# Performance work log

Hardware: AMD Instinct MI355X
Metric: run time of the kernel (lower is better)

Reference implementation:

```python
import jax, jax.numpy as jnp
import numpy as np

B, D, K = 65536, 128, 8
BOUND = 3.0
MIN_BIN_W = 1e-3   # min_bin_width
MIN_BIN_H = 1e-3   # min_bin_height
MIN_DERIV = 1e-3   # min_derivative
EPS = 1e-6


def setup_inputs() -> dict:
    key = jax.random.key(0)
    k1, k2, k3, k4 = jax.random.split(key, 4)
    return {
        "x": jax.random.normal(k1, (B, D), jnp.float32) * 1.5,
        "unnormalized_widths": jax.random.normal(k2, (D, K), jnp.float32),
        "unnormalized_heights": jax.random.normal(k3, (D, K), jnp.float32),
        "unnormalized_derivatives": jax.random.normal(k4, (D, K - 1), jnp.float32),
    }


def _calculate_knots(lengths, lower, upper):
    # lengths: [D, K] summing to ~1 -> scaled lengths and knot positions [D, K+1]
    knots = jnp.cumsum(lengths, axis=-1)
    knots = jnp.pad(knots, ((0, 0), (1, 0)))
    knots = (upper - lower) * knots + lower
    knots = knots.at[..., 0].set(lower)
    knots = knots.at[..., -1].set(upper)
    return knots[..., 1:] - knots[..., :-1], knots


def _select_bins(p, idx):
    # p: [D, Kp] per-dim tables, idx: [B, D] bin indices -> [B, D]
    i = jnp.clip(idx, 0, p.shape[-1] - 1)
    return p[jnp.arange(p.shape[0])[None, :], i]


def _spline_forward(x, uw, uh, ud):
    w = jax.nn.softmax(uw, axis=-1)
    h = jax.nn.softmax(uh, axis=-1)
    d = jax.nn.softplus(ud)

    num_bins = w.shape[-1]
    widths = MIN_BIN_W + (1.0 - MIN_BIN_W * num_bins) * w
    heights = MIN_BIN_H + (1.0 - MIN_BIN_H * num_bins) * h
    derivs = jnp.pad(MIN_DERIV + d, ((0, 0), (1, 1)), constant_values=1.0 - MIN_DERIV)  # [D, K+1]

    widths, cumwidths = _calculate_knots(widths, -BOUND, BOUND)
    heights, cumheights = _calculate_knots(heights, -BOUND, BOUND)

    inside = (x >= -BOUND) & (x <= BOUND)
    xc = jnp.clip(x, -BOUND, BOUND)  # keep tail values finite; masked out below

    # searchsorted: which bin each input falls into   [B, D]
    bin_idx = jnp.sum(xc[..., None] >= (cumwidths + EPS)[None, :, :], axis=-1) - 1

    iw = _select_bins(widths, bin_idx)
    icw = _select_bins(cumwidths, bin_idx)
    ich = _select_bins(cumheights, bin_idx)
    idelta = _select_bins(heights / widths, bin_idx)
    id0 = _select_bins(derivs, bin_idx)
    id1 = _select_bins(derivs[..., 1:], bin_idx)
    ih = _select_bins(heights, bin_idx)

    # rational quadratic spline (forward)
    theta = (xc - icw) / iw
    t1m = theta * (1.0 - theta)
    numerator = ih * (idelta * theta ** 2 + id0 * t1m)
    denominator = idelta + (id0 + id1 - 2.0 * idelta) * t1m
    out = ich + numerator / denominator
    dnum = idelta ** 2 * (id1 * theta ** 2 + 2.0 * idelta * t1m + id0 * (1.0 - theta) ** 2)
    lad = jnp.log(dnum) - 2.0 * jnp.log(denominator)

    u = jnp.where(inside, out, x)          # identity outside tail bound
    lad = jnp.where(inside, lad, 0.0)
    return u, lad


def reference(x, unnormalized_widths, unnormalized_heights, unnormalized_derivatives):
    u, lad = _spline_forward(x, unnormalized_widths, unnormalized_heights, unnormalized_derivatives)
    log_detJ = jnp.sum(lad, axis=1)
    return u, log_detJ
```

## Files before the change

### kernel.cpp

```cpp
#include <hip/hip_runtime.h>
#include <math.h>

namespace {
constexpr int D = 128;
constexpr int K = 8;
constexpr float BOUND = 3.0f;
constexpr float EPS = 1e-6f;
constexpr float MIN_BIN_W = 1e-3f;
constexpr float MIN_BIN_H = 1e-3f;
constexpr float MIN_DERIV = 1e-3f;
constexpr float LN2 = 0.6931471805599453f;
constexpr int WPB = 8;
constexpr int RPW = 8;
}

typedef float v2f __attribute__((ext_vector_type(2)));

template <int CTRL, int ROWM>
__device__ __forceinline__ float dpp_add(float v) {
    const int t = __builtin_amdgcn_update_dpp(0, __float_as_int(v), CTRL, ROWM, 0xf, true);
    return v + __int_as_float(t);
}

__device__ __forceinline__ float wave_sum_dpp(float v) {
    v = dpp_add<0x111, 0xf>(v);
    v = dpp_add<0x112, 0xf>(v);
    v = dpp_add<0x114, 0xf>(v);
    v = dpp_add<0x118, 0xf>(v);
    v = dpp_add<0x142, 0xa>(v);
    v = dpp_add<0x143, 0xc>(v);
    return v;
}

__global__ __launch_bounds__(512, 6) void spline_fwd(
    const float* __restrict__ x,
    const float* __restrict__ uw,
    const float* __restrict__ uh,
    const float* __restrict__ ud,
    float* __restrict__ out_u,
    float* __restrict__ out_ld,
    int nrows)
{
    __shared__ __align__(16) float4 s_T[2 * K * D];

    const int tid = threadIdx.x;
    if (tid < D) {
        const int d = tid;
        float wv[K], hv[K], cw[K + 1], ch[K + 1], der[K + 1];

        {
            const float* p = uw + d * K;
            float m = p[0];
            #pragma unroll
            for (int j = 1; j < K; ++j) m = fmaxf(m, p[j]);
            float s = 0.f;
            #pragma unroll
            for (int j = 0; j < K; ++j) { wv[j] = __expf(p[j] - m); s += wv[j]; }
            const float inv = (1.f - MIN_BIN_W * K) / s;
            #pragma unroll
            for (int j = 0; j < K; ++j) wv[j] = MIN_BIN_W + wv[j] * inv;
        }
        {
            const float* p = uh + d * K;
            float m = p[0];
            #pragma unroll
            for (int j = 1; j < K; ++j) m = fmaxf(m, p[j]);
            float s = 0.f;
            #pragma unroll
            for (int j = 0; j < K; ++j) { hv[j] = __expf(p[j] - m); s += hv[j]; }
            const float inv = (1.f - MIN_BIN_H * K) / s;
            #pragma unroll
            for (int j = 0; j < K; ++j) hv[j] = MIN_BIN_H + hv[j] * inv;
        }
        cw[0] = -BOUND; ch[0] = -BOUND;
        float cs_w = 0.f, cs_h = 0.f;
        #pragma unroll
        for (int j = 0; j < K; ++j) {
            cs_w += wv[j]; cw[j + 1] = 2.f * BOUND * cs_w - BOUND;
            cs_h += hv[j]; ch[j + 1] = 2.f * BOUND * cs_h - BOUND;
        }
        cw[K] = BOUND; ch[K] = BOUND;

        der[0] = 1.f - MIN_DERIV;
        der[K] = 1.f - MIN_DERIV;
        {
            const float* p = ud + d * (K - 1);
            #pragma unroll
            for (int j = 1; j < K; ++j) {
                const float v = p[j - 1];
                const float sp = log1pf(__expf(-fabsf(v))) + fmaxf(v, 0.f);
                der[j] = MIN_DERIV + sp;
            }
        }

        const int slot = (d & 1) * 64 + (d >> 1);
        #pragma unroll
        for (int j = 0; j < K; ++j) {
            const float w  = cw[j + 1] - cw[j];
            const float h  = ch[j + 1] - ch[j];
            const float iw = 1.f / w;
            const float dl = h * iw;
            s_T[j * D + slot] = make_float4(cw[j], iw, der[j], dl);
            s_T[K * D + j * D + slot] = make_float4(ch[j], h, der[j + 1],
                                                    der[j] + der[j + 1] - 2.f * dl);
        }
    }
    __syncthreads();

    const int wave = tid >> 6;
    const int lane = tid & 63;
    const int slot0 = lane;
    const int slot1 = 64 + lane;
    const float4* __restrict__ pa0 = s_T + slot0;
    const float4* __restrict__ pa1 = s_T + slot1;

    float kn0[7], kn1[7];
    #pragma unroll
    for (int j = 0; j < 7; ++j) {
        kn0[j] = pa0[(j + 1) * D].x + EPS;
        kn1[j] = pa1[(j + 1) * D].x + EPS;
    }

    const int r0 = (blockIdx.x * WPB + wave) * RPW;
    const int lo2 = lane * 2;
    const float* __restrict__ xbase = x + (size_t)r0 * D + lo2;
    float* __restrict__ ubase = out_u + (size_t)r0 * D + lo2;

    float2 xs[RPW];
    #pragma unroll
    for (int i = 0; i < RPW; ++i)
        xs[i] = *(const float2*)(xbase + (size_t)i * D);

    #pragma unroll
    for (int i = 0; i < RPW; ++i) {
        const float xv0 = xs[i].x, xv1 = xs[i].y;
        const float xc0 = fminf(fmaxf(xv0, -BOUND), BOUND);
        const float xc1 = fminf(fmaxf(xv1, -BOUND), BOUND);
        const bool in0 = fabsf(xv0) <= BOUND;
        const bool in1 = fabsf(xv1) <= BOUND;

        int i0 = 0, i1 = 0;
        #pragma unroll
        for (int j = 0; j < 7; ++j) {
            i0 += (xc0 >= kn0[j]) ? 1 : 0;
            i1 += (xc1 >= kn1[j]) ? 1 : 0;
        }

        const float4 ra0 = pa0[i0 * D];
        const float4 rb0 = pa0[i0 * D + K * D];
        const float4 ra1 = pa1[i1 * D];
        const float4 rb1 = pa1[i1 * D + K * D];

        const v2f xc  = {xc0, xc1};
        const v2f xw  = {xv0, xv1};
        const v2f icw = {ra0.x, ra1.x}, inw = {ra0.y, ra1.y};
        const v2f d0  = {ra0.z, ra1.z}, dl  = {ra0.w, ra1.w};
        const v2f ich = {rb0.x, rb1.x}, ih  = {rb0.y, rb1.y};
        const v2f d1  = {rb0.z, rb1.z}, E   = {rb0.w, rb1.w};

        const v2f theta = (xc - icw) * inw;
        const v2f omt   = (v2f)1.f - theta;
        const v2f t1m   = theta * omt;
        const v2f th2   = theta * theta;
        const v2f num   = ih * (dl * th2 + d0 * t1m);
        const v2f den   = dl + E * t1m;
        const v2f rd    = {__builtin_amdgcn_rcpf(den.x), __builtin_amdgcn_rcpf(den.y)};
        const v2f outv  = num * rd + ich;
        const v2f dnum  = (dl * dl) * (d1 * th2 + (dl + dl) * t1m + d0 * (omt * omt));
        const v2f P     = dnum * (rd * rd);

        const v2f u = outv + (xw - xc);
        *(float2*)(ubase + (size_t)i * D) = make_float2(u.x, u.y);

        const float P0 = in0 ? P.x : 1.f;
        const float P1 = in1 ? P.y : 1.f;
        float la = __log2f(P0 * P1);

        la = wave_sum_dpp(la);
        if (lane == 63) out_ld[r0 + i] = la * LN2;
    }
}

extern "C" void kernel_launch(void* const* d_in, const int* in_sizes, int n_in,
                              void* d_out, int out_size, void* d_ws, size_t ws_size,
                              hipStream_t stream) {
    const float* x  = (const float*)d_in[0];
    const float* uw = (const float*)d_in[1];
    const float* uh = (const float*)d_in[2];
    const float* ud = (const float*)d_in[3];
    const int nrows = in_sizes[0] / D;
    float* out_u  = (float*)d_out;
    float* out_ld = (float*)d_out + (size_t)nrows * D;
    const int nblocks = nrows / (WPB * RPW);
    spline_fwd<<<nblocks, 512, 0, stream>>>(x, uw, uh, ud, out_u, out_ld, nrows);
}
```

Measured before the change: 96.29 us.

## Process four dims per lane with float4 I/O and half-wave row reduction

Result: no change. 96.33 us (+0.0%).

```diff
diff --git a/kernel.cpp b/kernel.cpp
--- a/kernel.cpp
+++ b/kernel.cpp
@@ -22,17 +22,16 @@
     return v + __int_as_float(t);
 }
 
-__device__ __forceinline__ float wave_sum_dpp(float v) {
+__device__ __forceinline__ float half_sum_dpp(float v) {
     v = dpp_add<0x111, 0xf>(v);
     v = dpp_add<0x112, 0xf>(v);
     v = dpp_add<0x114, 0xf>(v);
     v = dpp_add<0x118, 0xf>(v);
     v = dpp_add<0x142, 0xa>(v);
-    v = dpp_add<0x143, 0xc>(v);
     return v;
 }
 
-__global__ __launch_bounds__(512, 6) void spline_fwd(
+__global__ __launch_bounds__(512, 4) void spline_fwd(
     const float* __restrict__ x,
     const float* __restrict__ uw,
     const float* __restrict__ uh,
@@ -93,7 +92,7 @@
             }
         }
 
-        const int slot = (d & 1) * 64 + (d >> 1);
+        const int slot = (d & 3) * 32 + (d >> 2);
         #pragma unroll
         for (int j = 0; j < K; ++j) {
             const float w  = cw[j + 1] - cw[j];
@@ -109,75 +108,90 @@
 
     const int wave = tid >> 6;
     const int lane = tid & 63;
-    const int slot0 = lane;
-    const int slot1 = 64 + lane;
-    const float4* __restrict__ pa0 = s_T + slot0;
-    const float4* __restrict__ pa1 = s_T + slot1;
-
-    float kn0[7], kn1[7];
+    const int l32  = lane & 31;
+    const int rsel = lane >> 5;
+
+    const float4* __restrict__ pa0 = s_T + (0 * 32 + l32);
+    const float4* __restrict__ pa1 = s_T + (1 * 32 + l32);
+    const float4* __restrict__ pa2 = s_T + (2 * 32 + l32);
+    const float4* __restrict__ pa3 = s_T + (3 * 32 + l32);
+
+    float kn0[7], kn1[7], kn2[7], kn3[7];
     #pragma unroll
     for (int j = 0; j < 7; ++j) {
         kn0[j] = pa0[(j + 1) * D].x + EPS;
         kn1[j] = pa1[(j + 1) * D].x + EPS;
+        kn2[j] = pa2[(j + 1) * D].x + EPS;
+        kn3[j] = pa3[(j + 1) * D].x + EPS;
     }
 
     const int r0 = (blockIdx.x * WPB + wave) * RPW;
-    const int lo2 = lane * 2;
-    const float* __restrict__ xbase = x + (size_t)r0 * D + lo2;
-    float* __restrict__ ubase = out_u + (size_t)r0 * D + lo2;
-
-    float2 xs[RPW];
+    const float* __restrict__ xbase = x + (size_t)(r0 + rsel) * D + l32 * 4;
+    float* __restrict__ ubase = out_u + (size_t)(r0 + rsel) * D + l32 * 4;
+
+    float4 xs[4];
     #pragma unroll
-    for (int i = 0; i < RPW; ++i)
-        xs[i] = *(const float2*)(xbase + (size_t)i * D);
+    for (int i = 0; i < 4; ++i)
+        xs[i] = *(const float4*)(xbase + (size_t)(2 * i) * D);
 
     #pragma unroll
-    for (int i = 0; i < RPW; ++i) {
-        const float xv0 = xs[i].x, xv1 = xs[i].y;
-        const float xc0 = fminf(fmaxf(xv0, -BOUND), BOUND);
-        const float xc1 = fminf(fmaxf(xv1, -BOUND), BOUND);
-        const bool in0 = fabsf(xv0) <= BOUND;
-        const bool in1 = fabsf(xv1) <= BOUND;
-
-        int i0 = 0, i1 = 0;
+    for (int i = 0; i < 4; ++i) {
+        const float4 xv = xs[i];
+        const float xc0 = fminf(fmaxf(xv.x, -BOUND), BOUND);
+        const float xc1 = fminf(fmaxf(xv.y, -BOUND), BOUND);
+        const float xc2 = fminf(fmaxf(xv.z, -BOUND), BOUND);
+        const float xc3 = fminf(fmaxf(xv.w, -BOUND), BOUND);
+
+        int i0 = 0, i1 = 0, i2 = 0, i3 = 0;
         #pragma unroll
         for (int j = 0; j < 7; ++j) {
             i0 += (xc0 >= kn0[j]) ? 1 : 0;
             i1 += (xc1 >= kn1[j]) ? 1 : 0;
-        }
-
-        const float4 ra0 = pa0[i0 * D];
-        const float4 rb0 = pa0[i0 * D + K * D];
-        const float4 ra1 = pa1[i1 * D];
-        const float4 rb1 = pa1[i1 * D + K * D];
-
-        const v2f xc  = {xc0, xc1};
-        const v2f xw  = {xv0, xv1};
-        const v2f icw = {ra0.x, ra1.x}, inw = {ra0.y, ra1.y};
-        const v2f d0  = {ra0.z, ra1.z}, dl  = {ra0.w, ra1.w};
-        const v2f ich = {rb0.x, rb1.x}, ih  = {rb0.y, rb1.y};
-        const v2f d1  = {rb0.z, rb1.z}, E   = {rb0.w, rb1.w};
-
-        const v2f theta = (xc - icw) * inw;
-        const v2f omt   = (v2f)1.f - theta;
-        const v2f t1m   = theta * omt;
-        const v2f th2   = theta * theta;
-        const v2f num   = ih * (dl * th2 + d0 * t1m);
-        const v2f den   = dl + E * t1m;
-        const v2f rd    = {__builtin_amdgcn_rcpf(den.x), __builtin_amdgcn_rcpf(den.y)};
-        const v2f outv  = num * rd + ich;
-        const v2f dnum  = (dl * dl) * (d1 * th2 + (dl + dl) * t1m + d0 * (omt * omt));
-        const v2f P     = dnum * (rd * rd);
-
-        const v2f u = outv + (xw - xc);
-        *(float2*)(ubase + (size_t)i * D) = make_float2(u.x, u.y);
-
-        const float P0 = in0 ? P.x : 1.f;
-        const float P1 = in1 ? P.y : 1.f;
-        float la = __log2f(P0 * P1);
-
-        la = wave_sum_dpp(la);
-        if (lane == 63) out_ld[r0 + i] = la * LN2;
+            i2 += (xc2 >= kn2[j]) ? 1 : 0;
+            i3 += (xc3 >= kn3[j]) ? 1 : 0;
+        }
+
+        const float4 ra0 = pa0[i0 * D], rb0 = pa0[i0 * D + K * D];
+        const float4 ra1 = pa1[i1 * D], rb1 = pa1[i1 * D + K * D];
+        const float4 ra2 = pa2[i2 * D], rb2 = pa2[i2 * D + K * D];
+        const float4 ra3 = pa3[i3 * D], rb3 = pa3[i3 * D + K * D];
+
+        const v2f xcA = {xc0, xc1},  xcB = {xc2, xc3};
+        const v2f xwA = {xv.x, xv.y}, xwB = {xv.z, xv.w};
+        const v2f icwA = {ra0.x, ra1.x}, icwB = {ra2.x, ra3.x};
+        const v2f inwA = {ra0.y, ra1.y}, inwB = {ra2.y, ra3.y};
+        const v2f d0A  = {ra0.z, ra1.z}, d0B  = {ra2.z, ra3.z};
+        const v2f dlA  = {ra0.w, ra1.w}, dlB  = {ra2.w, ra3.w};
+        const v2f ichA = {rb0.x, rb1.x}, ichB = {rb2.x, rb3.x};
+        const v2f ihA  = {rb0.y, rb1.y}, ihB  = {rb2.y, rb3.y};
+        const v2f d1A  = {rb0.z, rb1.z}, d1B  = {rb2.z, rb3.z};
+        const v2f EA   = {rb0.w, rb1.w}, EB   = {rb2.w, rb3.w};
+
+        const v2f thA = (xcA - icwA) * inwA,      thB = (xcB - icwB) * inwB;
+        const v2f omA = (v2f)1.f - thA,           omB = (v2f)1.f - thB;
+        const v2f tmA = thA * omA,                tmB = thB * omB;
+        const v2f t2A = thA * thA,                t2B = thB * thB;
+        const v2f nmA = ihA * (dlA * t2A + d0A * tmA);
+        const v2f nmB = ihB * (dlB * t2B + d0B * tmB);
+        const v2f dnA = dlA + EA * tmA,           dnB = dlB + EB * tmB;
+        const v2f rdA = {__builtin_amdgcn_rcpf(dnA.x), __builtin_amdgcn_rcpf(dnA.y)};
+        const v2f rdB = {__builtin_amdgcn_rcpf(dnB.x), __builtin_amdgcn_rcpf(dnB.y)};
+        const v2f ovA = nmA * rdA + ichA,         ovB = nmB * rdB + ichB;
+        const v2f duA = (dlA * dlA) * (d1A * t2A + (dlA + dlA) * tmA + d0A * (omA * omA));
+        const v2f duB = (dlB * dlB) * (d1B * t2B + (dlB + dlB) * tmB + d0B * (omB * omB));
+        const v2f PA  = duA * (rdA * rdA),        PB  = duB * (rdB * rdB);
+
+        const v2f uA = ovA + (xwA - xcA),         uB = ovB + (xwB - xcB);
+        *(float4*)(ubase + (size_t)(2 * i) * D) = make_float4(uA.x, uA.y, uB.x, uB.y);
+
+        const float P0 = (fabsf(xv.x) <= BOUND) ? PA.x : 1.f;
+        const float P1 = (fabsf(xv.y) <= BOUND) ? PA.y : 1.f;
+        const float P2 = (fabsf(xv.z) <= BOUND) ? PB.x : 1.f;
+        const float P3 = (fabsf(xv.w) <= BOUND) ? PB.y : 1.f;
+        float la = __log2f(P0 * P1) + __log2f(P2 * P3);
+
+        la = half_sum_dpp(la);
+        if (l32 == 31) out_ld[r0 + 2 * i + rsel] = la * LN2;
     }
 }
 
```
